# Kernel optimization log

Hardware: AMD Instinct MI355X
Metric: run time of the kernel (lower is better)

Reference implementation:

```python
import jax, jax.numpy as jnp
import numpy as np
import math

DIM = 1024
DIM_HEAD = 64
HEADS = 16
B, N = 2, 2048


def _layernorm(x, g, b, eps=1e-5):
    x32 = x.astype(jnp.float32)
    mu = jnp.mean(x32, axis=-1, keepdims=True)
    var = jnp.var(x32, axis=-1, keepdims=True)
    return ((x32 - mu) * jax.lax.rsqrt(var + eps) * g + b).astype(x.dtype)


def setup_inputs() -> dict:
    key = jax.random.key(0)
    ks = jax.random.split(key, 8)
    inner = DIM_HEAD * HEADS
    return {
        "x": jax.random.normal(ks[0], (B, N, DIM), dtype=jnp.float32),
        "w_q": jax.random.normal(ks[1], (inner, DIM), dtype=jnp.float32) * 0.02,
        "w_kv": jax.random.normal(ks[2], (2 * DIM_HEAD, DIM), dtype=jnp.float32) * 0.02,
        "w_out": jax.random.normal(ks[3], (DIM, inner), dtype=jnp.float32) * 0.02,
        "ln_g": jnp.ones((DIM,), dtype=jnp.float32),
        "ln_b": jnp.zeros((DIM,), dtype=jnp.float32),
        "lno_g": jnp.ones((DIM,), dtype=jnp.float32),
        "lno_b": jnp.zeros((DIM,), dtype=jnp.float32),
    }


def reference(x, w_q, w_kv, w_out, ln_g, ln_b, lno_g, lno_b):
    b, n, _ = x.shape
    scale = DIM_HEAD ** -0.5
    xn = _layernorm(x, ln_g, ln_b)
    q = jnp.einsum('bnc,ec->bne', xn, w_q)                 # [b, n, h*d]
    kv = jnp.einsum('bnc,ec->bne', xn, w_kv)               # [b, n, 2*d]
    k, v = jnp.split(kv, 2, axis=-1)                        # each [b, n, d]
    q = q.reshape(b, n, HEADS, DIM_HEAD).transpose(0, 2, 1, 3)  # [b, h, n, d]
    # faithful double scaling: q*scale then q,k each *sqrt(scale)
    sqs = math.sqrt(scale)
    q = q * (scale * sqs)
    k = k * sqs
    sim = jnp.einsum('bhid,bjd->bhij', q, k)                # [b, h, n, n]
    max_neg = -jnp.finfo(sim.dtype).max
    causal_mask = jnp.triu(jnp.ones((n, n), dtype=bool), k=1)
    sim = jnp.where(causal_mask, max_neg, sim)
    attn = jax.nn.softmax(sim.astype(jnp.float32), axis=-1).astype(sim.dtype)
    out = jnp.einsum('bhij,bjd->bhid', attn, v)             # [b, h, n, d]
    out = out.transpose(0, 2, 1, 3).reshape(b, n, HEADS * DIM_HEAD)
    out = jnp.einsum('bne,ce->bnc', out, w_out)             # [b, n, dim]
    return _layernorm(out, lno_g, lno_b)
```

## Files before the change

kernel.cpp:

```cpp
#include <hip/hip_runtime.h>
#include <hip/hip_bf16.h>
#include <stdint.h>

typedef unsigned short u16;
typedef __bf16 bf16x8 __attribute__((ext_vector_type(8)));
typedef float f32x4 __attribute__((ext_vector_type(4)));

#define MFMA16(a, b, c) __builtin_amdgcn_mfma_f32_16x16x32_bf16((a), (b), (c), 0, 0, 0)

#define BATCH 2
#define NSEQ 2048
#define DIMC 1024
#define NHEAD 16
#define DHEAD 64

__device__ __forceinline__ u16 f2bf(float f) {
  unsigned u = __float_as_uint(f);
  u += 0x7FFFu + ((u >> 16) & 1u);
  return (u16)(u >> 16);
}
__device__ __forceinline__ float bf2f(u16 h) {
  return __uint_as_float(((unsigned)h) << 16);
}
__device__ __forceinline__ void gload_lds16(const void* g, void* lds) {
  __builtin_amdgcn_global_load_lds((const __attribute__((address_space(1))) void*)g,
                                   (__attribute__((address_space(3))) void*)lds,
                                   16, 0, 0);
}
#define WAIT_VM(N) asm volatile("s_waitcnt vmcnt(" #N ")" ::: "memory")
#define BARRIER() __builtin_amdgcn_s_barrier()

__global__ __launch_bounds__(256) void cvt_f32_bf16(const float* __restrict__ in,
                                                    u16* __restrict__ out, int n) {
  int i = (blockIdx.x * 256 + threadIdx.x) * 4;
  if (i < n) {
    float4 v = *(const float4*)(in + i);
    ushort4 o;
    o.x = f2bf(v.x); o.y = f2bf(v.y); o.z = f2bf(v.z); o.w = f2bf(v.w);
    *(ushort4*)(out + i) = o;
  }
}

__global__ __launch_bounds__(256) void ln_f32_to_bf16(const float* __restrict__ X,
                                                      const float* __restrict__ G,
                                                      const float* __restrict__ Bv,
                                                      u16* __restrict__ Y) {
  const int row = blockIdx.x;
  const int tid = threadIdx.x;
  const float4 v = *(const float4*)(X + (size_t)row * DIMC + tid * 4);
  float s = v.x + v.y + v.z + v.w;
  float q = v.x * v.x + v.y * v.y + v.z * v.z + v.w * v.w;
#pragma unroll
  for (int d = 1; d < 64; d <<= 1) {
    s += __shfl_xor(s, d, 64);
    q += __shfl_xor(q, d, 64);
  }
  __shared__ float ps[4], pq[4];
  const int w = tid >> 6, l = tid & 63;
  if (l == 0) { ps[w] = s; pq[w] = q; }
  __syncthreads();
  s = ps[0] + ps[1] + ps[2] + ps[3];
  q = pq[0] + pq[1] + pq[2] + pq[3];
  const float mean = s * (1.f / DIMC);
  const float var = q * (1.f / DIMC) - mean * mean;
  const float rs = rsqrtf(var + 1e-5f);
  const float4 g = *(const float4*)(G + tid * 4);
  const float4 bb = *(const float4*)(Bv + tid * 4);
  ushort4 o;
  o.x = f2bf((v.x - mean) * rs * g.x + bb.x);
  o.y = f2bf((v.y - mean) * rs * g.y + bb.y);
  o.z = f2bf((v.z - mean) * rs * g.z + bb.z);
  o.w = f2bf((v.w - mean) * rs * g.w + bb.w);
  *(ushort4*)(Y + (size_t)row * DIMC + tid * 4) = o;
}

__global__ __launch_bounds__(256) void ln_bf16_to_f32(const u16* __restrict__ X,
                                                      const float* __restrict__ G,
                                                      const float* __restrict__ Bv,
                                                      float* __restrict__ Y) {
  const int row = blockIdx.x;
  const int tid = threadIdx.x;
  const ushort4 hv = *(const ushort4*)(X + (size_t)row * DIMC + tid * 4);
  float x0 = bf2f(hv.x), x1 = bf2f(hv.y), x2 = bf2f(hv.z), x3 = bf2f(hv.w);
  float s = x0 + x1 + x2 + x3;
  float q = x0 * x0 + x1 * x1 + x2 * x2 + x3 * x3;
#pragma unroll
  for (int d = 1; d < 64; d <<= 1) {
    s += __shfl_xor(s, d, 64);
    q += __shfl_xor(q, d, 64);
  }
  __shared__ float ps[4], pq[4];
  const int w = tid >> 6, l = tid & 63;
  if (l == 0) { ps[w] = s; pq[w] = q; }
  __syncthreads();
  s = ps[0] + ps[1] + ps[2] + ps[3];
  q = pq[0] + pq[1] + pq[2] + pq[3];
  const float mean = s * (1.f / DIMC);
  const float var = q * (1.f / DIMC) - mean * mean;
  const float rs = rsqrtf(var + 1e-5f);
  const float4 g = *(const float4*)(G + tid * 4);
  const float4 bb = *(const float4*)(Bv + tid * 4);
  float4 o;
  o.x = (x0 - mean) * rs * g.x + bb.x;
  o.y = (x1 - mean) * rs * g.y + bb.y;
  o.z = (x2 - mean) * rs * g.z + bb.z;
  o.w = (x3 - mean) * rs * g.w + bb.w;
  *(float4*)(Y + (size_t)row * DIMC + tid * 4) = o;
}

template <int MODE>
__global__ __launch_bounds__(256) void gemm_bt(const u16* __restrict__ A,
                                               const u16* __restrict__ Bw,
                                               u16* __restrict__ out0,
                                               u16* __restrict__ out1,
                                               u16* __restrict__ out2,
                                               int M, int N, int K, float scale0) {
  const int tid = threadIdx.x;
  const int w = tid >> 6, l = tid & 63;
  const int wr = w >> 1, wc = w & 1;
  const int lr = l & 15, lg = l >> 4;

  const int nwgx = gridDim.x;
  const int nwg = nwgx * gridDim.y;
  int flat = blockIdx.x + nwgx * blockIdx.y;
  if ((nwg & 7) == 0) flat = (flat & 7) * (nwg >> 3) + (flat >> 3);
  const int m0 = (flat / nwgx) * 128, n0 = (flat % nwgx) * 128;

  __shared__ u16 As[2][128 * 64];
  __shared__ u16 Bs[2][128 * 64];

  f32x4 acc[4][4] = {};

  auto STAGE = [&](int buf, int kt) {
#pragma unroll
    for (int r = 0; r < 4; ++r) {
      const int c = w * 4 + r;
      const int lo = c * 1024 + l * 16;
      const int row = lo >> 7;
      const int pb = lo & 127;
      const int cl = pb ^ ((row & 7) << 4);
      gload_lds16((const char*)A + ((size_t)(m0 + row) * K + kt * 64) * 2 + cl,
                  (char*)As[buf] + c * 1024);
      gload_lds16((const char*)Bw + ((size_t)(n0 + row) * K + kt * 64) * 2 + cl,
                  (char*)Bs[buf] + c * 1024);
    }
  };

  const int nk = K >> 6;
  STAGE(0, 0);
  if (nk > 1) STAGE(1, 1);
  int cur = 0;
  for (int kt = 0; kt < nk; ++kt) {
    if (kt + 1 < nk) { WAIT_VM(8); } else { WAIT_VM(0); }
    BARRIER();
    const char* as = (const char*)As[cur];
    const char* bs = (const char*)Bs[cur];
#pragma unroll
    for (int ks = 0; ks < 2; ++ks) {
      bf16x8 af[4], bfr[4];
#pragma unroll
      for (int mi = 0; mi < 4; ++mi) {
        const int row = wr * 64 + mi * 16 + lr;
        af[mi] = *(const bf16x8*)(as + row * 128 + ((ks * 64 + lg * 16) ^ ((row & 7) << 4)));
      }
#pragma unroll
      for (int ni = 0; ni < 4; ++ni) {
        const int row = wc * 64 + ni * 16 + lr;
        bfr[ni] = *(const bf16x8*)(bs + row * 128 + ((ks * 64 + lg * 16) ^ ((row & 7) << 4)));
      }
#pragma unroll
      for (int mi = 0; mi < 4; ++mi)
#pragma unroll
        for (int ni = 0; ni < 4; ++ni)
          acc[mi][ni] = MFMA16(af[mi], bfr[ni], acc[mi][ni]);
    }
    BARRIER();
    if (kt + 2 < nk) STAGE(cur, kt + 2);
    cur ^= 1;
  }

  if constexpr (MODE == 0) {
#pragma unroll
    for (int mi = 0; mi < 4; ++mi)
#pragma unroll
      for (int ni = 0; ni < 4; ++ni)
#pragma unroll
        for (int r = 0; r < 4; ++r) {
          const int row = m0 + wr * 64 + mi * 16 + lg * 4 + r;
          const int col = n0 + wc * 64 + ni * 16 + lr;
          out0[(size_t)row * N + col] = f2bf(acc[mi][ni][r] * scale0);
        }
  } else {
    const float sqs = 0.35355339059327379f;
#pragma unroll
    for (int mi = 0; mi < 4; ++mi)
#pragma unroll
      for (int ni = 0; ni < 4; ++ni)
#pragma unroll
        for (int r = 0; r < 4; ++r) {
          const int m = m0 + wr * 64 + mi * 16 + lg * 4 + r;
          const int col = n0 + wc * 64 + ni * 16 + lr;
          const float vv = acc[mi][ni][r];
          if (col < 1024) {
            out0[(size_t)m * 1024 + col] = f2bf(vv * scale0);
          } else {
            const int b = m >> 11, n = m & 2047;
            const int colk = col - 1024;
            if (colk < 64) {
              out1[(size_t)m * 64 + colk] = f2bf(vv * sqs);
            } else {
              const int d = colk - 64;
              out2[((size_t)b * 64 + d) * NSEQ + n] = f2bf(vv);
            }
          }
        }
  }
}

__global__ __launch_bounds__(256) void attn_causal(const u16* __restrict__ Q,
                                                   const u16* __restrict__ Kg,
                                                   const u16* __restrict__ VTg,
                                                   u16* __restrict__ O) {
  const int pi = blockIdx.x;
  const int qtA = pi, qtB = 31 - pi;
  const int bh = blockIdx.y;
  const int b = bh >> 4, h = bh & 15;
  const int tid = threadIdx.x;
  const int w = tid >> 6, l = tid & 63;
  const int lr = l & 15, lg = l >> 4;

  __shared__ u16 Ks[2][64 * 64];
  __shared__ u16 Vs[2][64 * 64];
  __shared__ u16 Ps[4][16 * 64];

  const int qrowA = qtA * 64 + w * 16 + lr;
  const int qrowB = qtB * 64 + w * 16 + lr;
  const size_t qbA = ((size_t)(b * NSEQ + qrowA)) * DIMC + h * DHEAD;
  const size_t qbB = ((size_t)(b * NSEQ + qrowB)) * DIMC + h * DHEAD;
  const bf16x8 aqA0 = *(const bf16x8*)(Q + qbA + lg * 8);
  const bf16x8 aqA1 = *(const bf16x8*)(Q + qbA + 32 + lg * 8);
  const bf16x8 aqB0 = *(const bf16x8*)(Q + qbB + lg * 8);
  const bf16x8 aqB1 = *(const bf16x8*)(Q + qbB + 32 + lg * 8);

  const char* kb = (const char*)(Kg + (size_t)b * NSEQ * DHEAD);
  const char* vb = (const char*)(VTg + (size_t)b * DHEAD * NSEQ);

  float mA[4], lA[4], mB[4], lB[4];
  f32x4 oA[4], oB[4];
#pragma unroll
  for (int r = 0; r < 4; ++r) { mA[r] = -1e30f; lA[r] = 0.f; mB[r] = -1e30f; lB[r] = 0.f; }
#pragma unroll
  for (int f = 0; f < 4; ++f) { oA[f] = f32x4{0.f,0.f,0.f,0.f}; oB[f] = f32x4{0.f,0.f,0.f,0.f}; }

  auto STAGE = [&](int buf, int kt) {
#pragma unroll
    for (int r = 0; r < 2; ++r) {
      const int c = w * 2 + r;
      const int lo = c * 1024 + l * 16;
      const int row = lo >> 7;
      const int pb = lo & 127;
      const int cl = pb ^ ((row & 7) << 4);
      gload_lds16(kb + (size_t)(kt * 64 + row) * 128 + cl, (char*)Ks[buf] + c * 1024);
      gload_lds16(vb + (size_t)row * (NSEQ * 2) + kt * 128 + cl, (char*)Vs[buf] + c * 1024);
    }
  };

  auto TILE = [&](const bf16x8 q0, const bf16x8 q1, float* mr, float* lsum,
                  f32x4* oa, int qt, int kt, int cur) {
    f32x4 s[4];
    __builtin_amdgcn_s_setprio(1);
#pragma unroll
    for (int f = 0; f < 4; ++f) {
      s[f] = f32x4{0.f, 0.f, 0.f, 0.f};
      const int krow = f * 16 + lr;
      const char* krp = (const char*)Ks[cur] + krow * 128;
      const int ksw = (krow & 7) << 4;
      const bf16x8 b0 = *(const bf16x8*)(krp + ((lg * 16) ^ ksw));
      const bf16x8 b1 = *(const bf16x8*)(krp + ((64 + lg * 16) ^ ksw));
      s[f] = MFMA16(q0, b0, s[f]);
      s[f] = MFMA16(q1, b1, s[f]);
    }
    __builtin_amdgcn_s_setprio(0);

    if (kt == qt) {
#pragma unroll
      for (int f = 0; f < 4; ++f)
#pragma unroll
        for (int r = 0; r < 4; ++r)
          if (f * 16 + lr > w * 16 + lg * 4 + r) s[f][r] = -1e30f;
    }

    float pr[4][4];
#pragma unroll
    for (int r = 0; r < 4; ++r) {
      float mx = fmaxf(fmaxf(s[0][r], s[1][r]), fmaxf(s[2][r], s[3][r]));
#pragma unroll
      for (int d = 1; d < 16; d <<= 1) mx = fmaxf(mx, __shfl_xor(mx, d, 64));
      const float mnew = fmaxf(mr[r], mx);
      const float sc = exp2f(mr[r] - mnew);
      float ls = 0.f;
#pragma unroll
      for (int f = 0; f < 4; ++f) {
        const float p = exp2f(s[f][r] - mnew);
        pr[f][r] = p;
        ls += p;
      }
#pragma unroll
      for (int d = 1; d < 16; d <<= 1) ls += __shfl_xor(ls, d, 64);
      lsum[r] = lsum[r] * sc + ls;
      mr[r] = mnew;
#pragma unroll
      for (int f = 0; f < 4; ++f) oa[f][r] *= sc;
    }

    u16* pw = &Ps[w][0];
#pragma unroll
    for (int f = 0; f < 4; ++f)
#pragma unroll
      for (int r = 0; r < 4; ++r) {
        const int row = lg * 4 + r;
        const int cbyte = (f * 16 + lr) * 2;
        *(u16*)((char*)pw + row * 128 + (cbyte ^ ((row & 7) << 4))) = f2bf(pr[f][r]);
      }

    const int psw = (lr & 7) << 4;
    const bf16x8 ap0 = *(const bf16x8*)((const char*)pw + lr * 128 + ((lg * 16) ^ psw));
    const bf16x8 ap1 = *(const bf16x8*)((const char*)pw + lr * 128 + ((64 + lg * 16) ^ psw));
    __builtin_amdgcn_s_setprio(1);
#pragma unroll
    for (int f = 0; f < 4; ++f) {
      const int vrow = f * 16 + lr;
      const char* vr = (const char*)Vs[cur] + vrow * 128;
      const int vsw = (vrow & 7) << 4;
      const bf16x8 b0 = *(const bf16x8*)(vr + ((lg * 16) ^ vsw));
      const bf16x8 b1 = *(const bf16x8*)(vr + ((64 + lg * 16) ^ vsw));
      oa[f] = MFMA16(ap0, b0, oa[f]);
      oa[f] = MFMA16(ap1, b1, oa[f]);
    }
    __builtin_amdgcn_s_setprio(0);
  };

  const int nkt = qtB + 1;
  STAGE(0, 0);
  STAGE(1, 1);
  int cur = 0;
  for (int kt = 0; kt < nkt; ++kt) {
    if (kt + 1 < nkt) { WAIT_VM(4); } else { WAIT_VM(0); }
    BARRIER();
    if (kt <= qtA) TILE(aqA0, aqA1, mA, lA, oA, qtA, kt, cur);
    TILE(aqB0, aqB1, mB, lB, oB, qtB, kt, cur);
    BARRIER();
    if (kt + 2 < nkt) STAGE(cur, kt + 2);
    cur ^= 1;
  }

  float invA[4], invB[4];
#pragma unroll
  for (int r = 0; r < 4; ++r) { invA[r] = 1.f / lA[r]; invB[r] = 1.f / lB[r]; }
#pragma unroll
  for (int f = 0; f < 4; ++f)
#pragma unroll
    for (int r = 0; r < 4; ++r) {
      const int col = h * DHEAD + f * 16 + lr;
      const int rowA = qtA * 64 + w * 16 + lg * 4 + r;
      O[((size_t)(b * NSEQ + rowA)) * DIMC + col] = f2bf(oA[f][r] * invA[r]);
      const int rowB = qtB * 64 + w * 16 + lg * 4 + r;
      O[((size_t)(b * NSEQ + rowB)) * DIMC + col] = f2bf(oB[f][r] * invB[r]);
    }
}

extern "C" void kernel_launch(void* const* d_in, const int* in_sizes, int n_in,
                              void* d_out, int out_size, void* d_ws, size_t ws_size,
                              hipStream_t stream) {
  const float* x = (const float*)d_in[0];
  const float* w_q = (const float*)d_in[1];
  const float* w_kv = (const float*)d_in[2];
  const float* w_out = (const float*)d_in[3];
  const float* ln_g = (const float*)d_in[4];
  const float* ln_b = (const float*)d_in[5];
  const float* lno_g = (const float*)d_in[6];
  const float* lno_b = (const float*)d_in[7];
  float* out = (float*)d_out;

  char* ws = (char*)d_ws;
  size_t off = 0;
  auto alloc = [&](size_t bytes) {
    char* p = ws + off;
    off += (bytes + 255) & ~(size_t)255;
    return p;
  };
  u16* xn    = (u16*)alloc((size_t)BATCH * NSEQ * DIMC * 2);
  u16* wqkv  = (u16*)alloc((size_t)1152 * DIMC * 2);
  u16* wob   = (u16*)alloc((size_t)DIMC * DIMC * 2);
  u16* qb    = (u16*)alloc((size_t)BATCH * NSEQ * DIMC * 2);
  u16* kb    = (u16*)alloc((size_t)BATCH * NSEQ * DHEAD * 2);
  u16* vtb   = (u16*)alloc((size_t)BATCH * DHEAD * NSEQ * 2);
  u16* ao = xn;
  u16* yb = qb;

  const float qscale = (float)(0.044194173824159216 * 1.4426950408889634);

  cvt_f32_bf16<<<1024, 256, 0, stream>>>(w_q, wqkv, DIMC * DIMC);
  cvt_f32_bf16<<<128, 256, 0, stream>>>(w_kv, wqkv + (size_t)DIMC * DIMC, 128 * DIMC);
  cvt_f32_bf16<<<1024, 256, 0, stream>>>(w_out, wob, DIMC * DIMC);

  ln_f32_to_bf16<<<BATCH * NSEQ, 256, 0, stream>>>(x, ln_g, ln_b, xn);

  gemm_bt<2><<<dim3(9, 32), 256, 0, stream>>>(xn, wqkv, qb, kb, vtb,
                                              BATCH * NSEQ, 1152, DIMC, qscale);

  attn_causal<<<dim3(16, 32), 256, 0, stream>>>(qb, kb, vtb, ao);

  gemm_bt<0><<<dim3(8, 32), 256, 0, stream>>>(ao, wob, yb, nullptr, nullptr,
                                              BATCH * NSEQ, DIMC, DIMC, 1.f);

  ln_bf16_to_f32<<<BATCH * NSEQ, 256, 0, stream>>>(yb, lno_g, lno_b, out);
}
```

Measured before the change: 210.7 us.

## Use 8-wave GEMM blocks and 128-key attention tiles with lazy rescaling

The GEMM moves to 512 threads with a 2x4 wave grid, so each wave computes a 64x32 sub-tile. Its MFMA loop is wrapped in setprio, and the grid swizzle is now applied unconditionally. The attention kernel now processes 128-key tiles, halving barrier and loop iterations per query tile. It also skips the online-softmax rescale unless the running max grows by more than a threshold, and truncates P to bf16 instead of rounding it. These changes trade extra registers and LDS, plus slight numeric differences from lazy rescaling and truncation, for less synchronization and less softmax overhead.

Result: faster. 201.9 us (-4.2%).

```diff
diff --git a/kernel.cpp b/kernel.cpp
--- a/kernel.cpp
+++ b/kernel.cpp
@@ -109,7 +109,7 @@
 }
 
 template <int MODE>
-__global__ __launch_bounds__(256) void gemm_bt(const u16* __restrict__ A,
+__global__ __launch_bounds__(512) void gemm_bt(const u16* __restrict__ A,
                                                const u16* __restrict__ Bw,
                                                u16* __restrict__ out0,
                                                u16* __restrict__ out1,
@@ -117,28 +117,27 @@
                                                int M, int N, int K, float scale0) {
   const int tid = threadIdx.x;
   const int w = tid >> 6, l = tid & 63;
-  const int wr = w >> 1, wc = w & 1;
+  const int wr = w >> 2, wc = w & 3;
   const int lr = l & 15, lg = l >> 4;
 
   const int nwgx = gridDim.x;
   const int nwg = nwgx * gridDim.y;
   int flat = blockIdx.x + nwgx * blockIdx.y;
-  if ((nwg & 7) == 0) flat = (flat & 7) * (nwg >> 3) + (flat >> 3);
+  flat = (flat & 7) * (nwg >> 3) + (flat >> 3);
   const int m0 = (flat / nwgx) * 128, n0 = (flat % nwgx) * 128;
 
   __shared__ u16 As[2][128 * 64];
   __shared__ u16 Bs[2][128 * 64];
 
-  f32x4 acc[4][4] = {};
+  f32x4 acc[4][2] = {};
 
   auto STAGE = [&](int buf, int kt) {
 #pragma unroll
-    for (int r = 0; r < 4; ++r) {
-      const int c = w * 4 + r;
+    for (int r = 0; r < 2; ++r) {
+      const int c = w * 2 + r;
       const int lo = c * 1024 + l * 16;
       const int row = lo >> 7;
-      const int pb = lo & 127;
-      const int cl = pb ^ ((row & 7) << 4);
+      const int cl = (lo & 127) ^ ((row & 7) << 4);
       gload_lds16((const char*)A + ((size_t)(m0 + row) * K + kt * 64) * 2 + cl,
                   (char*)As[buf] + c * 1024);
       gload_lds16((const char*)Bw + ((size_t)(n0 + row) * K + kt * 64) * 2 + cl,
@@ -148,31 +147,33 @@
 
   const int nk = K >> 6;
   STAGE(0, 0);
-  if (nk > 1) STAGE(1, 1);
+  STAGE(1, 1);
   int cur = 0;
   for (int kt = 0; kt < nk; ++kt) {
-    if (kt + 1 < nk) { WAIT_VM(8); } else { WAIT_VM(0); }
+    if (kt + 1 < nk) { WAIT_VM(4); } else { WAIT_VM(0); }
     BARRIER();
     const char* as = (const char*)As[cur];
     const char* bs = (const char*)Bs[cur];
 #pragma unroll
     for (int ks = 0; ks < 2; ++ks) {
-      bf16x8 af[4], bfr[4];
+      bf16x8 af[4], bfr[2];
 #pragma unroll
       for (int mi = 0; mi < 4; ++mi) {
         const int row = wr * 64 + mi * 16 + lr;
         af[mi] = *(const bf16x8*)(as + row * 128 + ((ks * 64 + lg * 16) ^ ((row & 7) << 4)));
       }
 #pragma unroll
-      for (int ni = 0; ni < 4; ++ni) {
-        const int row = wc * 64 + ni * 16 + lr;
+      for (int ni = 0; ni < 2; ++ni) {
+        const int row = wc * 32 + ni * 16 + lr;
         bfr[ni] = *(const bf16x8*)(bs + row * 128 + ((ks * 64 + lg * 16) ^ ((row & 7) << 4)));
       }
+      __builtin_amdgcn_s_setprio(1);
 #pragma unroll
       for (int mi = 0; mi < 4; ++mi)
 #pragma unroll
-        for (int ni = 0; ni < 4; ++ni)
+        for (int ni = 0; ni < 2; ++ni)
           acc[mi][ni] = MFMA16(af[mi], bfr[ni], acc[mi][ni]);
+      __builtin_amdgcn_s_setprio(0);
     }
     BARRIER();
     if (kt + 2 < nk) STAGE(cur, kt + 2);
@@ -183,11 +184,11 @@
 #pragma unroll
     for (int mi = 0; mi < 4; ++mi)
 #pragma unroll
-      for (int ni = 0; ni < 4; ++ni)
+      for (int ni = 0; ni < 2; ++ni)
 #pragma unroll
         for (int r = 0; r < 4; ++r) {
           const int row = m0 + wr * 64 + mi * 16 + lg * 4 + r;
-          const int col = n0 + wc * 64 + ni * 16 + lr;
+          const int col = n0 + wc * 32 + ni * 16 + lr;
           out0[(size_t)row * N + col] = f2bf(acc[mi][ni][r] * scale0);
         }
   } else {
@@ -195,11 +196,11 @@
 #pragma unroll
     for (int mi = 0; mi < 4; ++mi)
 #pragma unroll
-      for (int ni = 0; ni < 4; ++ni)
+      for (int ni = 0; ni < 2; ++ni)
 #pragma unroll
         for (int r = 0; r < 4; ++r) {
           const int m = m0 + wr * 64 + mi * 16 + lg * 4 + r;
-          const int col = n0 + wc * 64 + ni * 16 + lr;
+          const int col = n0 + wc * 32 + ni * 16 + lr;
           const float vv = acc[mi][ni][r];
           if (col < 1024) {
             out0[(size_t)m * 1024 + col] = f2bf(vv * scale0);
@@ -229,9 +230,9 @@
   const int w = tid >> 6, l = tid & 63;
   const int lr = l & 15, lg = l >> 4;
 
-  __shared__ u16 Ks[2][64 * 64];
-  __shared__ u16 Vs[2][64 * 64];
-  __shared__ u16 Ps[4][16 * 64];
+  __shared__ u16 Ks[2][128 * 64];
+  __shared__ u16 Vs[2][64 * 128];
+  __shared__ u16 Ps[4][16 * 128];
 
   const int qrowA = qtA * 64 + w * 16 + lr;
   const int qrowB = qtB * 64 + w * 16 + lr;
@@ -252,25 +253,26 @@
 #pragma unroll
   for (int f = 0; f < 4; ++f) { oA[f] = f32x4{0.f,0.f,0.f,0.f}; oB[f] = f32x4{0.f,0.f,0.f,0.f}; }
 
-  auto STAGE = [&](int buf, int kt) {
-#pragma unroll
-    for (int r = 0; r < 2; ++r) {
-      const int c = w * 2 + r;
+  auto STAGE = [&](int buf, int ktv) {
+#pragma unroll
+    for (int r = 0; r < 4; ++r) {
+      const int c = w * 4 + r;
       const int lo = c * 1024 + l * 16;
-      const int row = lo >> 7;
-      const int pb = lo & 127;
-      const int cl = pb ^ ((row & 7) << 4);
-      gload_lds16(kb + (size_t)(kt * 64 + row) * 128 + cl, (char*)Ks[buf] + c * 1024);
-      gload_lds16(vb + (size_t)row * (NSEQ * 2) + kt * 128 + cl, (char*)Vs[buf] + c * 1024);
+      const int krow = lo >> 7;
+      const int kcl = (lo & 127) ^ ((krow & 7) << 4);
+      gload_lds16(kb + (size_t)(ktv * 128 + krow) * 128 + kcl, (char*)Ks[buf] + c * 1024);
+      const int vrow = lo >> 8;
+      const int vcl = (lo & 255) ^ ((vrow & 7) << 4);
+      gload_lds16(vb + (size_t)vrow * (NSEQ * 2) + ktv * 256 + vcl, (char*)Vs[buf] + c * 1024);
     }
   };
 
   auto TILE = [&](const bf16x8 q0, const bf16x8 q1, float* mr, float* lsum,
-                  f32x4* oa, int qt, int kt, int cur) {
-    f32x4 s[4];
+                  f32x4* oa, int qt, int ktv, int cur) {
+    f32x4 s[8];
     __builtin_amdgcn_s_setprio(1);
 #pragma unroll
-    for (int f = 0; f < 4; ++f) {
+    for (int f = 0; f < 8; ++f) {
       s[f] = f32x4{0.f, 0.f, 0.f, 0.f};
       const int krow = f * 16 + lr;
       const char* krp = (const char*)Ks[cur] + krow * 128;
@@ -282,75 +284,94 @@
     }
     __builtin_amdgcn_s_setprio(0);
 
-    if (kt == qt) {
-#pragma unroll
-      for (int f = 0; f < 4; ++f)
+    if (ktv == (qt >> 1)) {
+#pragma unroll
+      for (int f = 0; f < 8; ++f)
 #pragma unroll
         for (int r = 0; r < 4; ++r)
-          if (f * 16 + lr > w * 16 + lg * 4 + r) s[f][r] = -1e30f;
-    }
-
-    float pr[4][4];
+          if (ktv * 128 + f * 16 + lr > qt * 64 + w * 16 + lg * 4 + r) s[f][r] = -1e30f;
+    }
+
+    float mx[4];
 #pragma unroll
     for (int r = 0; r < 4; ++r) {
-      float mx = fmaxf(fmaxf(s[0][r], s[1][r]), fmaxf(s[2][r], s[3][r]));
-#pragma unroll
-      for (int d = 1; d < 16; d <<= 1) mx = fmaxf(mx, __shfl_xor(mx, d, 64));
-      const float mnew = fmaxf(mr[r], mx);
-      const float sc = exp2f(mr[r] - mnew);
+      float m0_ = fmaxf(fmaxf(s[0][r], s[1][r]), fmaxf(s[2][r], s[3][r]));
+      float m1_ = fmaxf(fmaxf(s[4][r], s[5][r]), fmaxf(s[6][r], s[7][r]));
+      float v = fmaxf(m0_, m1_);
+#pragma unroll
+      for (int d = 1; d < 16; d <<= 1) v = fmaxf(v, __shfl_xor(v, d, 64));
+      mx[r] = v;
+    }
+    const bool grow = (mx[0] - mr[0] > 6.f) || (mx[1] - mr[1] > 6.f) ||
+                      (mx[2] - mr[2] > 6.f) || (mx[3] - mr[3] > 6.f);
+    if (__any(grow)) {
+#pragma unroll
+      for (int r = 0; r < 4; ++r) {
+        const float mnew = fmaxf(mr[r], mx[r]);
+        const float sc = exp2f(mr[r] - mnew);
+        lsum[r] *= sc;
+        mr[r] = mnew;
+#pragma unroll
+        for (int f = 0; f < 4; ++f) oa[f][r] *= sc;
+      }
+    }
+#pragma unroll
+    for (int r = 0; r < 4; ++r) {
       float ls = 0.f;
 #pragma unroll
-      for (int f = 0; f < 4; ++f) {
-        const float p = exp2f(s[f][r] - mnew);
-        pr[f][r] = p;
+      for (int f = 0; f < 8; ++f) {
+        const float p = exp2f(s[f][r] - mr[r]);
+        s[f][r] = p;
         ls += p;
       }
 #pragma unroll
       for (int d = 1; d < 16; d <<= 1) ls += __shfl_xor(ls, d, 64);
-      lsum[r] = lsum[r] * sc + ls;
-      mr[r] = mnew;
-#pragma unroll
-      for (int f = 0; f < 4; ++f) oa[f][r] *= sc;
+      lsum[r] += ls;
     }
 
     u16* pw = &Ps[w][0];
 #pragma unroll
-    for (int f = 0; f < 4; ++f)
+    for (int f = 0; f < 8; ++f)
 #pragma unroll
       for (int r = 0; r < 4; ++r) {
         const int row = lg * 4 + r;
         const int cbyte = (f * 16 + lr) * 2;
-        *(u16*)((char*)pw + row * 128 + (cbyte ^ ((row & 7) << 4))) = f2bf(pr[f][r]);
+        *(u16*)((char*)pw + row * 256 + (cbyte ^ ((row & 7) << 4))) =
+            (u16)(__float_as_uint(s[f][r]) >> 16);
       }
 
     const int psw = (lr & 7) << 4;
-    const bf16x8 ap0 = *(const bf16x8*)((const char*)pw + lr * 128 + ((lg * 16) ^ psw));
-    const bf16x8 ap1 = *(const bf16x8*)((const char*)pw + lr * 128 + ((64 + lg * 16) ^ psw));
+    bf16x8 ap[4];
+#pragma unroll
+    for (int ks = 0; ks < 4; ++ks)
+      ap[ks] = *(const bf16x8*)((const char*)pw + lr * 256 + ((ks * 64 + lg * 16) ^ psw));
     __builtin_amdgcn_s_setprio(1);
 #pragma unroll
     for (int f = 0; f < 4; ++f) {
       const int vrow = f * 16 + lr;
-      const char* vr = (const char*)Vs[cur] + vrow * 128;
+      const char* vr = (const char*)Vs[cur] + vrow * 256;
       const int vsw = (vrow & 7) << 4;
-      const bf16x8 b0 = *(const bf16x8*)(vr + ((lg * 16) ^ vsw));
-      const bf16x8 b1 = *(const bf16x8*)(vr + ((64 + lg * 16) ^ vsw));
-      oa[f] = MFMA16(ap0, b0, oa[f]);
-      oa[f] = MFMA16(ap1, b1, oa[f]);
+#pragma unroll
+      for (int ks = 0; ks < 4; ++ks) {
+        const bf16x8 vf = *(const bf16x8*)(vr + ((ks * 64 + lg * 16) ^ vsw));
+        oa[f] = MFMA16(ap[ks], vf, oa[f]);
+      }
     }
     __builtin_amdgcn_s_setprio(0);
   };
 
-  const int nkt = qtB + 1;
+  const int nkt = (qtB >> 1) + 1;
+  const int lastA = qtA >> 1;
   STAGE(0, 0);
   STAGE(1, 1);
   int cur = 0;
-  for (int kt = 0; kt < nkt; ++kt) {
-    if (kt + 1 < nkt) { WAIT_VM(4); } else { WAIT_VM(0); }
+  for (int ktv = 0; ktv < nkt; ++ktv) {
+    if (ktv + 1 < nkt) { WAIT_VM(8); } else { WAIT_VM(0); }
     BARRIER();
-    if (kt <= qtA) TILE(aqA0, aqA1, mA, lA, oA, qtA, kt, cur);
-    TILE(aqB0, aqB1, mB, lB, oB, qtB, kt, cur);
+    if (ktv <= lastA) TILE(aqA0, aqA1, mA, lA, oA, qtA, ktv, cur);
+    TILE(aqB0, aqB1, mB, lB, oB, qtB, ktv, cur);
     BARRIER();
-    if (kt + 2 < nkt) STAGE(cur, kt + 2);
+    if (ktv + 2 < nkt) STAGE(cur, ktv + 2);
     cur ^= 1;
   }
 
@@ -406,12 +427,12 @@
 
   ln_f32_to_bf16<<<BATCH * NSEQ, 256, 0, stream>>>(x, ln_g, ln_b, xn);
 
-  gemm_bt<2><<<dim3(9, 32), 256, 0, stream>>>(xn, wqkv, qb, kb, vtb,
+  gemm_bt<2><<<dim3(9, 32), 512, 0, stream>>>(xn, wqkv, qb, kb, vtb,
                                               BATCH * NSEQ, 1152, DIMC, qscale);
 
   attn_causal<<<dim3(16, 32), 256, 0, stream>>>(qb, kb, vtb, ao);
 
-  gemm_bt<0><<<dim3(8, 32), 256, 0, stream>>>(ao, wob, yb, nullptr, nullptr,
+  gemm_bt<0><<<dim3(8, 32), 512, 0, stream>>>(ao, wob, yb, nullptr, nullptr,
                                               BATCH * NSEQ, DIMC, DIMC, 1.f);
 
   ln_bf16_to_f32<<<BATCH * NSEQ, 256, 0, stream>>>(yb, lno_g, lno_b, out);
```

## Widen GEMM to 8 waves, add lazy softmax rescale and truncating P conversion

Applied to the files above, without the earlier changes.

The projection GEMMs now run 512 threads per block as 8 waves, each computing a 64x32 sub-tile, with MFMA priority hints, to raise occupancy and latency hiding. The attention softmax rescales its running max only when a row max grows by more than a threshold, skipping exp and accumulator scaling on most tiles. P values are converted to bf16 by truncation instead of rounding. The attention K/V pipeline becomes issue-next-then-compute with __syncthreads in place of explicit vmcnt waits. Together these trade exactness of rounding and a possible change in load overlap for less ALU work per tile.

Result: no change. 211.4 us (+0.3%).

```diff
diff --git a/kernel.cpp b/kernel.cpp
--- a/kernel.cpp
+++ b/kernel.cpp
@@ -109,36 +109,35 @@
 }
 
 template <int MODE>
-__global__ __launch_bounds__(256) void gemm_bt(const u16* __restrict__ A,
-                                               const u16* __restrict__ Bw,
-                                               u16* __restrict__ out0,
-                                               u16* __restrict__ out1,
-                                               u16* __restrict__ out2,
-                                               int M, int N, int K, float scale0) {
+__global__ __launch_bounds__(512, 4) void gemm_bt(const u16* __restrict__ A,
+                                                  const u16* __restrict__ Bw,
+                                                  u16* __restrict__ out0,
+                                                  u16* __restrict__ out1,
+                                                  u16* __restrict__ out2,
+                                                  int M, int N, int K, float scale0) {
   const int tid = threadIdx.x;
   const int w = tid >> 6, l = tid & 63;
-  const int wr = w >> 1, wc = w & 1;
+  const int wr = w >> 2, wc = w & 3;
   const int lr = l & 15, lg = l >> 4;
 
   const int nwgx = gridDim.x;
   const int nwg = nwgx * gridDim.y;
   int flat = blockIdx.x + nwgx * blockIdx.y;
-  if ((nwg & 7) == 0) flat = (flat & 7) * (nwg >> 3) + (flat >> 3);
+  flat = (flat & 7) * (nwg >> 3) + (flat >> 3);
   const int m0 = (flat / nwgx) * 128, n0 = (flat % nwgx) * 128;
 
   __shared__ u16 As[2][128 * 64];
   __shared__ u16 Bs[2][128 * 64];
 
-  f32x4 acc[4][4] = {};
+  f32x4 acc[4][2] = {};
 
   auto STAGE = [&](int buf, int kt) {
 #pragma unroll
-    for (int r = 0; r < 4; ++r) {
-      const int c = w * 4 + r;
+    for (int r = 0; r < 2; ++r) {
+      const int c = w * 2 + r;
       const int lo = c * 1024 + l * 16;
       const int row = lo >> 7;
-      const int pb = lo & 127;
-      const int cl = pb ^ ((row & 7) << 4);
+      const int cl = (lo & 127) ^ ((row & 7) << 4);
       gload_lds16((const char*)A + ((size_t)(m0 + row) * K + kt * 64) * 2 + cl,
                   (char*)As[buf] + c * 1024);
       gload_lds16((const char*)Bw + ((size_t)(n0 + row) * K + kt * 64) * 2 + cl,
@@ -148,31 +147,33 @@
 
   const int nk = K >> 6;
   STAGE(0, 0);
-  if (nk > 1) STAGE(1, 1);
+  STAGE(1, 1);
   int cur = 0;
   for (int kt = 0; kt < nk; ++kt) {
-    if (kt + 1 < nk) { WAIT_VM(8); } else { WAIT_VM(0); }
+    if (kt + 1 < nk) { WAIT_VM(4); } else { WAIT_VM(0); }
     BARRIER();
     const char* as = (const char*)As[cur];
     const char* bs = (const char*)Bs[cur];
 #pragma unroll
     for (int ks = 0; ks < 2; ++ks) {
-      bf16x8 af[4], bfr[4];
+      bf16x8 af[4], bfr[2];
 #pragma unroll
       for (int mi = 0; mi < 4; ++mi) {
         const int row = wr * 64 + mi * 16 + lr;
         af[mi] = *(const bf16x8*)(as + row * 128 + ((ks * 64 + lg * 16) ^ ((row & 7) << 4)));
       }
 #pragma unroll
-      for (int ni = 0; ni < 4; ++ni) {
-        const int row = wc * 64 + ni * 16 + lr;
+      for (int ni = 0; ni < 2; ++ni) {
+        const int row = wc * 32 + ni * 16 + lr;
         bfr[ni] = *(const bf16x8*)(bs + row * 128 + ((ks * 64 + lg * 16) ^ ((row & 7) << 4)));
       }
+      __builtin_amdgcn_s_setprio(1);
 #pragma unroll
       for (int mi = 0; mi < 4; ++mi)
 #pragma unroll
-        for (int ni = 0; ni < 4; ++ni)
+        for (int ni = 0; ni < 2; ++ni)
           acc[mi][ni] = MFMA16(af[mi], bfr[ni], acc[mi][ni]);
+      __builtin_amdgcn_s_setprio(0);
     }
     BARRIER();
     if (kt + 2 < nk) STAGE(cur, kt + 2);
@@ -183,11 +184,11 @@
 #pragma unroll
     for (int mi = 0; mi < 4; ++mi)
 #pragma unroll
-      for (int ni = 0; ni < 4; ++ni)
+      for (int ni = 0; ni < 2; ++ni)
 #pragma unroll
         for (int r = 0; r < 4; ++r) {
           const int row = m0 + wr * 64 + mi * 16 + lg * 4 + r;
-          const int col = n0 + wc * 64 + ni * 16 + lr;
+          const int col = n0 + wc * 32 + ni * 16 + lr;
           out0[(size_t)row * N + col] = f2bf(acc[mi][ni][r] * scale0);
         }
   } else {
@@ -195,11 +196,11 @@
 #pragma unroll
     for (int mi = 0; mi < 4; ++mi)
 #pragma unroll
-      for (int ni = 0; ni < 4; ++ni)
+      for (int ni = 0; ni < 2; ++ni)
 #pragma unroll
         for (int r = 0; r < 4; ++r) {
           const int m = m0 + wr * 64 + mi * 16 + lg * 4 + r;
-          const int col = n0 + wc * 64 + ni * 16 + lr;
+          const int col = n0 + wc * 32 + ni * 16 + lr;
           const float vv = acc[mi][ni][r];
           if (col < 1024) {
             out0[(size_t)m * 1024 + col] = f2bf(vv * scale0);
@@ -258,8 +259,7 @@
       const int c = w * 2 + r;
       const int lo = c * 1024 + l * 16;
       const int row = lo >> 7;
-      const int pb = lo & 127;
-      const int cl = pb ^ ((row & 7) << 4);
+      const int cl = (lo & 127) ^ ((row & 7) << 4);
       gload_lds16(kb + (size_t)(kt * 64 + row) * 128 + cl, (char*)Ks[buf] + c * 1024);
       gload_lds16(vb + (size_t)row * (NSEQ * 2) + kt * 128 + cl, (char*)Vs[buf] + c * 1024);
     }
@@ -290,27 +290,39 @@
           if (f * 16 + lr > w * 16 + lg * 4 + r) s[f][r] = -1e30f;
     }
 
-    float pr[4][4];
+    float mx[4];
 #pragma unroll
     for (int r = 0; r < 4; ++r) {
-      float mx = fmaxf(fmaxf(s[0][r], s[1][r]), fmaxf(s[2][r], s[3][r]));
-#pragma unroll
-      for (int d = 1; d < 16; d <<= 1) mx = fmaxf(mx, __shfl_xor(mx, d, 64));
-      const float mnew = fmaxf(mr[r], mx);
-      const float sc = exp2f(mr[r] - mnew);
+      float v = fmaxf(fmaxf(s[0][r], s[1][r]), fmaxf(s[2][r], s[3][r]));
+#pragma unroll
+      for (int d = 1; d < 16; d <<= 1) v = fmaxf(v, __shfl_xor(v, d, 64));
+      mx[r] = v;
+    }
+    const bool grow = (mx[0] - mr[0] > 6.f) || (mx[1] - mr[1] > 6.f) ||
+                      (mx[2] - mr[2] > 6.f) || (mx[3] - mr[3] > 6.f);
+    if (__any(grow)) {
+#pragma unroll
+      for (int r = 0; r < 4; ++r) {
+        const float mnew = fmaxf(mr[r], mx[r]);
+        const float sc = exp2f(mr[r] - mnew);
+        lsum[r] *= sc;
+        mr[r] = mnew;
+#pragma unroll
+        for (int f = 0; f < 4; ++f) oa[f][r] *= sc;
+      }
+    }
+#pragma unroll
+    for (int r = 0; r < 4; ++r) {
       float ls = 0.f;
 #pragma unroll
       for (int f = 0; f < 4; ++f) {
-        const float p = exp2f(s[f][r] - mnew);
-        pr[f][r] = p;
+        const float p = exp2f(s[f][r] - mr[r]);
+        s[f][r] = p;
         ls += p;
       }
 #pragma unroll
       for (int d = 1; d < 16; d <<= 1) ls += __shfl_xor(ls, d, 64);
-      lsum[r] = lsum[r] * sc + ls;
-      mr[r] = mnew;
-#pragma unroll
-      for (int f = 0; f < 4; ++f) oa[f][r] *= sc;
+      lsum[r] += ls;
     }
 
     u16* pw = &Ps[w][0];
@@ -320,7 +332,8 @@
       for (int r = 0; r < 4; ++r) {
         const int row = lg * 4 + r;
         const int cbyte = (f * 16 + lr) * 2;
-        *(u16*)((char*)pw + row * 128 + (cbyte ^ ((row & 7) << 4))) = f2bf(pr[f][r]);
+        *(u16*)((char*)pw + row * 128 + (cbyte ^ ((row & 7) << 4))) =
+            (u16)(__float_as_uint(s[f][r]) >> 16);
       }
 
     const int psw = (lr & 7) << 4;
@@ -342,15 +355,13 @@
 
   const int nkt = qtB + 1;
   STAGE(0, 0);
-  STAGE(1, 1);
+  __syncthreads();
   int cur = 0;
   for (int kt = 0; kt < nkt; ++kt) {
-    if (kt + 1 < nkt) { WAIT_VM(4); } else { WAIT_VM(0); }
-    BARRIER();
+    if (kt + 1 < nkt) STAGE(cur ^ 1, kt + 1);
     if (kt <= qtA) TILE(aqA0, aqA1, mA, lA, oA, qtA, kt, cur);
     TILE(aqB0, aqB1, mB, lB, oB, qtB, kt, cur);
-    BARRIER();
-    if (kt + 2 < nkt) STAGE(cur, kt + 2);
+    __syncthreads();
     cur ^= 1;
   }
 
@@ -406,12 +417,12 @@
 
   ln_f32_to_bf16<<<BATCH * NSEQ, 256, 0, stream>>>(x, ln_g, ln_b, xn);
 
-  gemm_bt<2><<<dim3(9, 32), 256, 0, stream>>>(xn, wqkv, qb, kb, vtb,
+  gemm_bt<2><<<dim3(9, 32), 512, 0, stream>>>(xn, wqkv, qb, kb, vtb,
                                               BATCH * NSEQ, 1152, DIMC, qscale);
 
   attn_causal<<<dim3(16, 32), 256, 0, stream>>>(qb, kb, vtb, ao);
 
-  gemm_bt<0><<<dim3(8, 32), 256, 0, stream>>>(ao, wob, yb, nullptr, nullptr,
+  gemm_bt<0><<<dim3(8, 32), 512, 0, stream>>>(ao, wob, yb, nullptr, nullptr,
                                               BATCH * NSEQ, DIMC, DIMC, 1.f);
 
   ln_bf16_to_f32<<<BATCH * NSEQ, 256, 0, stream>>>(yb, lno_g, lno_b, out);
```
